# Optimization experiments

Hardware: AMD Instinct MI355X
Metric: run time of the kernel (lower is better)

## Reference

```python
import jax, jax.numpy as jnp
import numpy as np

TEMPERATURE = 0.1  # base_temperature=0.07 is unused in the original forward
K = 100            # hard-coded top-k in the original forward


def setup_inputs() -> dict:
    key = jax.random.key(0)
    k1, k2, k3, k4 = jax.random.split(key, 4)
    B, T, D, N = 16, 2048, 256, 128
    context_feature = jax.random.normal(k1, (B, T, D), dtype=jnp.float32)
    target_feature = jax.random.normal(k2, (B, T, D), dtype=jnp.float32)
    # torch.unique(mask_index): supply a pre-uniqued sorted 1D index set directly
    mask_index = jnp.sort(jax.random.permutation(k3, T)[:N]).astype(jnp.int32)
    phone_label = jax.random.randint(k4, (B, T), 0, 100, dtype=jnp.int32)
    return {"context_feature": context_feature, "target_feature": target_feature,
            "mask_index": mask_index, "phone_label": phone_label}


def reference(context_feature, target_feature, mask_index, phone_label):
    B, T, D = context_feature.shape
    N = mask_index.shape[0]

    # phone gather + inequality mask (BN, BT)
    phone_n = phone_label[:, mask_index].reshape(B * N)
    phone_t = phone_label.reshape(B * T)
    neq_mask = (phone_n[:, None] != phone_t[None, :]).astype(context_feature.dtype)

    anchors = context_feature[:, mask_index, :].reshape(B * N, D)
    negative = target_feature.reshape(B * T, D)
    positive = target_feature[:, mask_index, :].reshape(B * N, D)

    a_norm = jnp.linalg.norm(anchors, axis=1)   # (BN,)
    p_norm = jnp.linalg.norm(positive, axis=1)  # (BN,)
    n_norm = jnp.linalg.norm(negative, axis=1)  # (BT,)

    # numerator: original builds full (BN,BN) cosine matrix but only uses diag;
    # compute the diagonal directly (identical math, far less memory)
    cos_pos = jnp.sum(anchors * positive, axis=1) / (a_norm * p_norm)
    sim_numerator = jnp.exp(jnp.arccos(jnp.clip(cos_pos, -1.0, 1.0)) / TEMPERATURE)

    # denominator: (BN, BT) cosine -> acos -> exp -> mask -> top-k sum
    cos_neg = (anchors @ negative.T) / (a_norm[:, None] * n_norm[None, :])
    sim_den = jnp.exp(jnp.arccos(jnp.clip(cos_neg, -1.0, 1.0)) / TEMPERATURE) * neq_mask
    top_vals = jax.lax.top_k(sim_den, K)[0]          # == sort desc then take first K
    sim_den_final = top_vals.sum(axis=1)             # (BN,)

    logit = jnp.log(sim_numerator / sim_den_final)
    loss = (-1.0 / (N * B)) * logit.sum()
    return loss
```

## Files before the change

### kernel.cpp

```cpp
#include <hip/hip_runtime.h>
#include <math.h>

#define TT 2048
#define TD 256
#define BN 2048
#define BT 32768
#define KTOP 100
#define CAP 1024
#define LCAP 1024
#define THETA -0.15f
#define BROWS 128
#define SLICE 512
#define NITER 16
#define FSCALE 301.176470588f
#define GH 32

typedef __attribute__((ext_vector_type(8))) short short8v;
typedef __attribute__((ext_vector_type(4))) float float4v;

__device__ __forceinline__ unsigned short f2bf(float f) {
    unsigned u = __float_as_uint(f);
    u += 0x7fffu + ((u >> 16) & 1u);
    return (unsigned short)(u >> 16);
}

__device__ __forceinline__ int tile_off_us(int col, int l) {
    int ks = l >> 3;
    int g = (l >> 1) & 3;
    int e = (l & 1) * 4;
    return ((((col >> 4) * 8 + ks) * 4 + g) * 16 + (col & 15)) * 8 + e;
}

__global__ __launch_bounds__(256) void kinit(const float* __restrict__ ctx,
                                             const float* __restrict__ tgt,
                                             const int* __restrict__ mask_index,
                                             const int* __restrict__ phone,
                                             unsigned short* __restrict__ negT,
                                             unsigned short* __restrict__ ancT,
                                             float* __restrict__ acosP,
                                             int* __restrict__ phoneA,
                                             unsigned* __restrict__ ghp,
                                             int* __restrict__ cnt,
                                             int* __restrict__ flagA) {
    const int bid = blockIdx.x;
    const int tid = threadIdx.x;

    if (bid < 2048) {
        __shared__ float tile[16][257];
        __shared__ float psum[16][8];
        __shared__ float inv[16];
        const int cb = bid;
        for (int r = 0; r < 16; ++r)
            tile[r][tid] = tgt[((size_t)cb * 16 + r) * TD + tid];
        __syncthreads();
        if (tid < 128) {
            int row = tid >> 3, seg = tid & 7;
            float s = 0.f;
            for (int j = 0; j < 32; ++j) {
                float x = tile[row][seg * 32 + j];
                s += x * x;
            }
            psum[row][seg] = s;
        }
        __syncthreads();
        if (tid < 16) {
            float s = 0.f;
            for (int j = 0; j < 8; ++j) s += psum[tid][j];
            inv[tid] = 1.0f / sqrtf(s);
        }
        __syncthreads();
        const int col = tid & 15;
        const float iv = inv[col];
        unsigned short* out = negT + (size_t)cb * 4096;
#pragma unroll
        for (int half = 0; half < 2; ++half) {
            const int d0 = (tid >> 4) * 8 + half * 128;
            ushort4 o0, o1;
            o0.x = f2bf(tile[col][d0 + 0] * iv);
            o0.y = f2bf(tile[col][d0 + 1] * iv);
            o0.z = f2bf(tile[col][d0 + 2] * iv);
            o0.w = f2bf(tile[col][d0 + 3] * iv);
            o1.x = f2bf(tile[col][d0 + 4] * iv);
            o1.y = f2bf(tile[col][d0 + 5] * iv);
            o1.z = f2bf(tile[col][d0 + 6] * iv);
            o1.w = f2bf(tile[col][d0 + 7] * iv);
            *reinterpret_cast<ushort4*>(out + (size_t)(half * 256 + tid) * 8) = o0;
            *reinterpret_cast<ushort4*>(out + (size_t)(half * 256 + tid) * 8 + 4) = o1;
        }
        return;
    }
    if (bid < 2560) {
        const int r = (bid - 2048) * 4 + (tid >> 6);
        const int lane = tid & 63;
        const int b = r >> 7;
        const int n = r & 127;
        const int t = mask_index[n];
        const size_t base = ((size_t)b * TT + t) * TD;
        float4 a = *reinterpret_cast<const float4*>(ctx + base + lane * 4);
        float4 p = *reinterpret_cast<const float4*>(tgt + base + lane * 4);
        float sa = a.x * a.x + a.y * a.y + a.z * a.z + a.w * a.w;
        float sp = p.x * p.x + p.y * p.y + p.z * p.z + p.w * p.w;
        float dp = a.x * p.x + a.y * p.y + a.z * p.z + a.w * p.w;
        for (int off = 32; off > 0; off >>= 1) {
            sa += __shfl_down(sa, off, 64);
            sp += __shfl_down(sp, off, 64);
            dp += __shfl_down(dp, off, 64);
        }
        sa = __shfl(sa, 0, 64);
        sp = __shfl(sp, 0, 64);
        dp = __shfl(dp, 0, 64);
        const float an = sqrtf(sa);
        const float inva = 1.0f / an;
        if (lane == 0) {
            float cp = dp / (an * sqrtf(sp));
            cp = fminf(1.f, fmaxf(-1.f, cp));
            acosP[r] = acosf(cp) * 10.0f;
            phoneA[r] = phone[b * TT + t];
        }
        ushort4 o;
        o.x = f2bf(a.x * inva); o.y = f2bf(a.y * inva);
        o.z = f2bf(a.z * inva); o.w = f2bf(a.w * inva);
        *reinterpret_cast<ushort4*>(ancT + tile_off_us(r, lane)) = o;
        return;
    }
    if (bid < 2560 + GH) {
        __shared__ unsigned h[128];
        const int s = bid - 2560;
        if (tid < 128) h[tid] = 0u;
        __syncthreads();
        const int base = s * (BT / GH);
        for (int i = tid; i < BT / GH; i += 256)
            atomicAdd(&h[phone[base + i] & 127], 1u);
        __syncthreads();
        if (tid < 128) ghp[s * 128 + tid] = h[tid];
        return;
    }
    {
        const int i = (bid - 2592) * 256 + tid;
        if (i < BN) { cnt[i] = 0; flagA[i] = 0; }
    }
}

__global__ __launch_bounds__(512, 4) void kpass(const short8v* __restrict__ ancT8,
                                                const short8v* __restrict__ negT8,
                                                const int* __restrict__ phoneT,
                                                const int* __restrict__ phoneA,
                                                float* __restrict__ list,
                                                int* __restrict__ cnt,
                                                int* __restrict__ flag) {
    __shared__ float candV[LCAP];
    __shared__ int candR[LCAP];
    __shared__ int s_nc;
    const int tid = threadIdx.x;
    const int w = tid >> 6;
    const int lane = tid & 63;
    const int g = lane >> 4;
    const int c = lane & 15;
    const int wr = w >> 1;
    const int wc = w & 1;
    const int logical = (blockIdx.x & 7) * 128 + (blockIdx.x >> 3);
    const int ct = logical >> 4;
    const int rt = logical & 15;
    const int row0 = rt * BROWS;
    const int colbase = ct * SLICE;

    if (tid == 0) s_nc = 0;

    short8v af[2][8];
#pragma unroll
    for (int mt = 0; mt < 2; ++mt) {
        const int tile = rt * 8 + wr * 2 + mt;
#pragma unroll
        for (int ks = 0; ks < 8; ++ks)
            af[mt][ks] = ancT8[(tile * 8 + ks) * 64 + lane];
    }
    int phA_r[2][4];
#pragma unroll
    for (int mt = 0; mt < 2; ++mt)
#pragma unroll
        for (int j = 0; j < 4; ++j)
            phA_r[mt][j] = phoneA[row0 + wr * 32 + mt * 16 + g * 4 + j];
    __syncthreads();

#pragma unroll 2
    for (int it = 0; it < NITER; ++it) {
        const int cb = colbase + it * 32 + wc * 16;
        const int fb = (cb >> 4) * 8 * 64 + lane;
        short8v bf[8];
#pragma unroll
        for (int ks = 0; ks < 8; ++ks)
            bf[ks] = negT8[fb + ks * 64];
        const int ph = phoneT[cb + c];
        float4v acc0 = (float4v){0.f, 0.f, 0.f, 0.f};
        float4v acc1 = (float4v){0.f, 0.f, 0.f, 0.f};
        __builtin_amdgcn_s_setprio(1);
#pragma unroll
        for (int ks = 0; ks < 8; ++ks) {
            acc0 = __builtin_amdgcn_mfma_f32_16x16x32_bf16(af[0][ks], bf[ks], acc0, 0, 0, 0);
            acc1 = __builtin_amdgcn_mfma_f32_16x16x32_bf16(af[1][ks], bf[ks], acc1, 0, 0, 0);
        }
        __builtin_amdgcn_s_setprio(0);
#pragma unroll
        for (int j = 0; j < 4; ++j) {
            float v0 = fminf(1.f, fmaxf(-1.f, acc0[j]));
            if (v0 < THETA && ph != phA_r[0][j]) {
                int k = atomicAdd(&s_nc, 1);
                if (k < LCAP) {
                    candV[k] = v0;
                    candR[k] = row0 + wr * 32 + g * 4 + j;
                }
            }
            float v1 = fminf(1.f, fmaxf(-1.f, acc1[j]));
            if (v1 < THETA && ph != phA_r[1][j]) {
                int k = atomicAdd(&s_nc, 1);
                if (k < LCAP) {
                    candV[k] = v1;
                    candR[k] = row0 + wr * 32 + 16 + g * 4 + j;
                }
            }
        }
    }

    __syncthreads();
    const int nc = s_nc;
    if (nc > LCAP) {
        for (int i = tid; i < BROWS; i += 512) flag[row0 + i] = 1;
    } else {
        for (int i = tid; i < nc; i += 512) {
            const int r = candR[i];
            int idx = atomicAdd(&cnt[r], 1);
            if (idx < CAP) list[(size_t)r * CAP + idx] = candV[i];
        }
    }
}

__global__ __launch_bounds__(64) void kfinal(const float* __restrict__ list,
                                             const int* __restrict__ cnt,
                                             const int* __restrict__ phoneA,
                                             const unsigned* __restrict__ ghp,
                                             const float* __restrict__ acosP,
                                             float* __restrict__ logits,
                                             int* __restrict__ flag) {
    __shared__ float sl[CAP];
    __shared__ unsigned subh[256];
    __shared__ float l2[128];
    __shared__ int s_b, s_cum, s_l2c;
    const int row = blockIdx.x;
    const int lane = threadIdx.x;
    const int mp = phoneA[row] & 127;
    int un = BT;
    for (int s = 0; s < GH; ++s) un -= (int)ghp[s * 128 + mp];
    const int kp = un < KTOP ? un : KTOP;
    const int c = cnt[row];
    if (kp <= 0) { if (lane == 0) logits[row] = acosP[row]; return; }
    if (c < kp || c > CAP) { if (lane == 0) flag[row] = 1; return; }

    for (int i = lane; i < c; i += 64) sl[i] = list[(size_t)row * CAP + i];
    for (int i = lane; i < 256; i += 64) subh[i] = 0u;
    if (lane == 0) s_l2c = 0;
    __syncthreads();

    for (int i = lane; i < c; i += 64) {
        int sb = (int)((sl[i] + 1.0f) * FSCALE);
        sb = sb < 0 ? 0 : (sb > 255 ? 255 : sb);
        atomicAdd(&subh[sb], 1u);
    }
    __syncthreads();
    if (lane == 0) {
        unsigned cum = 0;
        int b = 0;
        for (; b < 256; ++b) {
            if (cum + subh[b] >= (unsigned)kp) break;
            cum += subh[b];
        }
        s_b = b > 255 ? 255 : b;
        s_cum = (int)cum;
    }
    __syncthreads();
    const int bs = s_b, cum = s_cum;

    float ls = 0.f;
    for (int i = lane; i < c; i += 64) {
        float v = sl[i];
        int sb = (int)((v + 1.0f) * FSCALE);
        sb = sb < 0 ? 0 : (sb > 255 ? 255 : sb);
        if (sb < bs) {
            ls += expf(acosf(fminf(1.f, fmaxf(-1.f, v))) * 10.0f);
        } else if (sb == bs) {
            int k = atomicAdd(&s_l2c, 1);
            if (k < 128) l2[k] = v;
        }
    }
#pragma unroll
    for (int off = 1; off < 64; off <<= 1) ls += __shfl_xor(ls, off, 64);
    __syncthreads();
    const int n2 = s_l2c;
    if (n2 > 128) { if (lane == 0) flag[row] = 1; return; }

    float den = ls;
    int rem = kp - cum;
    if (rem > n2) rem = n2;
    float v0 = lane < n2 ? l2[lane] : 1e30f;
    float v1 = lane + 64 < n2 ? l2[lane + 64] : 1e30f;
    for (int it = 0; it < rem; ++it) {
        float mv = fminf(v0, v1);
        int mi = (v1 < v0) ? lane + 64 : lane;
#pragma unroll
        for (int off = 1; off < 64; off <<= 1) {
            float ov = __shfl_xor(mv, off, 64);
            int oi = __shfl_xor(mi, off, 64);
            if (ov < mv || (ov == mv && oi < mi)) { mv = ov; mi = oi; }
        }
        den += expf(acosf(fminf(1.f, fmaxf(-1.f, mv))) * 10.0f);
        if (mi == lane) v0 = 1e30f;
        if (mi == lane + 64) v1 = 1e30f;
    }
    if (lane == 0) logits[row] = acosP[row] - logf(den);
}

__global__ __launch_bounds__(256) void kfallback(const float* __restrict__ ctx,
                                                 const float* __restrict__ tgt,
                                                 const int* __restrict__ mask_index,
                                                 const int* __restrict__ phone,
                                                 const int* __restrict__ flag,
                                                 const unsigned* __restrict__ ghp,
                                                 const float* __restrict__ acosP,
                                                 float* __restrict__ logits) {
    const int row = blockIdx.x;
    if (!flag[row]) return;
    __shared__ float anc[TD];
    __shared__ float redf[256];
    __shared__ int redi[256];
    __shared__ unsigned hist[2048];
    __shared__ float lst[512];
    __shared__ int s_b, s_cum, s_lc;
    const int tid = threadIdx.x;
    const int b = row >> 7;
    const int t = mask_index[row & 127];
    const int mp = phone[b * TT + t];

    {
        float x = ctx[((size_t)b * TT + t) * TD + tid];
        redf[tid] = x * x;
        anc[tid] = x;
        __syncthreads();
        for (int s = 128; s > 0; s >>= 1) {
            if (tid < s) redf[tid] += redf[tid + s];
            __syncthreads();
        }
        float inv = 1.0f / sqrtf(redf[0]);
        __syncthreads();
        anc[tid] *= inv;
    }
    for (int i = tid; i < 2048; i += 256) hist[i] = 0u;
    if (tid == 0) s_lc = 0;
    __syncthreads();

    int un = BT;
    for (int s = 0; s < GH; ++s) un -= (int)ghp[s * 128 + (mp & 127)];
    const int kp = un < KTOP ? un : KTOP;
    if (kp <= 0) { if (tid == 0) logits[row] = acosP[row]; return; }

    for (int col = tid; col < BT; col += 256) {
        if (phone[col] == mp) continue;
        const float* nr = tgt + (size_t)col * TD;
        float dot = 0.f, sq = 0.f;
        for (int d = 0; d < TD; d += 4) {
            float4 v = *reinterpret_cast<const float4*>(nr + d);
            dot += anc[d] * v.x + anc[d + 1] * v.y + anc[d + 2] * v.z + anc[d + 3] * v.w;
            sq += v.x * v.x + v.y * v.y + v.z * v.z + v.w * v.w;
        }
        float cv = fminf(1.f, fmaxf(-1.f, dot / sqrtf(sq)));
        int bb = (int)((cv + 1.0f) * 1024.0f);
        bb = bb > 2047 ? 2047 : bb;
        atomicAdd(&hist[bb], 1u);
    }
    __syncthreads();
    if (tid == 0) {
        unsigned cum = 0;
        int bb = 0;
        for (; bb < 2048; ++bb) {
            if (cum + hist[bb] >= (unsigned)kp) break;
            cum += hist[bb];
        }
        s_b = bb > 2047 ? 2047 : bb;
        s_cum = (int)cum;
    }
    __syncthreads();
    const int bs = s_b;

    float ls = 0.f;
    for (int col = tid; col < BT; col += 256) {
        if (phone[col] == mp) continue;
        const float* nr = tgt + (size_t)col * TD;
        float dot = 0.f, sq = 0.f;
        for (int d = 0; d < TD; d += 4) {
            float4 v = *reinterpret_cast<const float4*>(nr + d);
            dot += anc[d] * v.x + anc[d + 1] * v.y + anc[d + 2] * v.z + anc[d + 3] * v.w;
            sq += v.x * v.x + v.y * v.y + v.z * v.z + v.w * v.w;
        }
        float cv = fminf(1.f, fmaxf(-1.f, dot / sqrtf(sq)));
        int bb = (int)((cv + 1.0f) * 1024.0f);
        bb = bb > 2047 ? 2047 : bb;
        if (bb < bs) {
            ls += expf(acosf(cv) * 10.0f);
        } else if (bb == bs) {
            int k = atomicAdd(&s_lc, 1);
            if (k < 512) lst[k] = cv;
        }
    }
    redf[tid] = ls;
    __syncthreads();
    for (int s = 128; s > 0; s >>= 1) {
        if (tid < s) redf[tid] += redf[tid + s];
        __syncthreads();
    }
    float den = redf[0];
    __syncthreads();

    int lc = s_lc < 512 ? s_lc : 512;
    int rem = kp - s_cum;
    if (rem > lc) rem = lc;
    for (int it = 0; it < rem; ++it) {
        float mv = 1e30f;
        int mi = -1;
        for (int i = tid; i < lc; i += 256) {
            if (lst[i] < mv) { mv = lst[i]; mi = i; }
        }
        redf[tid] = mv;
        redi[tid] = mi;
        __syncthreads();
        for (int s = 128; s > 0; s >>= 1) {
            if (tid < s && (redf[tid + s] < redf[tid] ||
                            (redf[tid + s] == redf[tid] && redi[tid + s] >= 0 &&
                             (redi[tid] < 0 || redi[tid + s] < redi[tid])))) {
                redf[tid] = redf[tid + s];
                redi[tid] = redi[tid + s];
            }
            __syncthreads();
        }
        if (tid == 0) {
            den += expf(acosf(fminf(1.f, fmaxf(-1.f, redf[0]))) * 10.0f);
            if (redi[0] >= 0) lst[redi[0]] = 1e30f;
            redf[0] = den;
        }
        __syncthreads();
        den = redf[0];
        __syncthreads();
    }
    if (tid == 0) logits[row] = acosP[row] - logf(den);
}

__global__ __launch_bounds__(256) void kloss(const float* __restrict__ logits,
                                             float* __restrict__ out) {
    __shared__ float red[256];
    int tid = threadIdx.x;
    float s = 0.f;
    for (int i = tid; i < BN; i += 256) s += logits[i];
    red[tid] = s;
    __syncthreads();
    for (int st = 128; st > 0; st >>= 1) {
        if (tid < st) red[tid] += red[tid + st];
        __syncthreads();
    }
    if (tid == 0) out[0] = -red[0] / (float)BN;
}

extern "C" void kernel_launch(void* const* d_in, const int* in_sizes, int n_in,
                              void* d_out, int out_size, void* d_ws, size_t ws_size,
                              hipStream_t stream) {
    (void)in_sizes; (void)n_in; (void)out_size; (void)ws_size;
    const float* ctx   = (const float*)d_in[0];
    const float* tgt   = (const float*)d_in[1];
    const int*   mask  = (const int*)d_in[2];
    const int*   phone = (const int*)d_in[3];
    float* out = (float*)d_out;

    char* p = (char*)d_ws;
    unsigned short* negT = (unsigned short*)p;            p += (size_t)BT * TD * 2;
    unsigned short* ancT = (unsigned short*)p;            p += (size_t)BN * TD * 2;
    float* acosP  = (float*)p;                            p += (size_t)BN * 4;
    int*   phoneA = (int*)p;                              p += (size_t)BN * 4;
    int*   cntA   = (int*)p;                              p += (size_t)BN * 4;
    int*   flagA  = (int*)p;                              p += (size_t)BN * 4;
    unsigned* ghp = (unsigned*)p;                         p += (size_t)GH * 128 * 4;
    float* listA  = (float*)p;                            p += (size_t)BN * CAP * 4;
    float* logits = (float*)p;                            p += (size_t)BN * 4;

    kinit<<<2600, 256, 0, stream>>>(ctx, tgt, mask, phone, negT, ancT,
                                    acosP, phoneA, ghp, cntA, flagA);
    kpass<<<1024, 512, 0, stream>>>((const short8v*)ancT, (const short8v*)negT,
                                    phone, phoneA, listA, cntA, flagA);
    kfinal<<<BN, 64, 0, stream>>>(listA, cntA, phoneA, ghp, acosP, logits, flagA);
    kfallback<<<BN, 256, 0, stream>>>(ctx, tgt, mask, phone, flagA, ghp, acosP, logits);
    kloss<<<1, 256, 0, stream>>>(logits, out);
}
```

Measured before the change: 132.9 us.

## Retile kpass: stage anchor tile in LDS via direct loads, widen column tiles

Changes the kpass tiling from 128 rows x 512 columns with 8 waves holding anchor fragments in registers to 64 rows x 1024 columns with 4 waves. The anchor tile is copied into LDS with global_load_lds, and each wave reads it from there for all four 16-row subtiles while reusing two negative fragments from registers. This raises reuse of each negative load and lowers register pressure, at the cost of LDS reads in the inner MFMA loop and more LDS per block. It also drops the redundant upper clamp, since only values below a negative threshold are kept.

```diff
diff --git a/kernel.cpp b/kernel.cpp
--- a/kernel.cpp
+++ b/kernel.cpp
@@ -9,9 +9,9 @@
 #define CAP 1024
 #define LCAP 1024
 #define THETA -0.15f
-#define BROWS 128
-#define SLICE 512
-#define NITER 16
+#define BROWS 64
+#define BCOLS 1024
+#define NITER 8
 #define FSCALE 301.176470588f
 #define GH 32
 
@@ -29,6 +29,12 @@
     int g = (l >> 1) & 3;
     int e = (l & 1) * 4;
     return ((((col >> 4) * 8 + ks) * 4 + g) * 16 + (col & 15)) * 8 + e;
+}
+
+__device__ __forceinline__ void gload16(const void* g, void* l) {
+    __builtin_amdgcn_global_load_lds(
+        (const __attribute__((address_space(1))) unsigned*)g,
+        (__attribute__((address_space(3))) unsigned*)l, 16, 0, 0);
 }
 
 __global__ __launch_bounds__(256) void kinit(const float* __restrict__ ctx,
@@ -141,13 +147,14 @@
     }
 }
 
-__global__ __launch_bounds__(512, 4) void kpass(const short8v* __restrict__ ancT8,
+__global__ __launch_bounds__(256, 3) void kpass(const short8v* __restrict__ ancT8,
                                                 const short8v* __restrict__ negT8,
                                                 const int* __restrict__ phoneT,
                                                 const int* __restrict__ phoneA,
                                                 float* __restrict__ list,
                                                 int* __restrict__ cnt,
                                                 int* __restrict__ flag) {
+    __shared__ short8v aLDS[2048];
     __shared__ float candV[LCAP];
     __shared__ int candR[LCAP];
     __shared__ int s_nc;
@@ -156,77 +163,79 @@
     const int lane = tid & 63;
     const int g = lane >> 4;
     const int c = lane & 15;
-    const int wr = w >> 1;
-    const int wc = w & 1;
     const int logical = (blockIdx.x & 7) * 128 + (blockIdx.x >> 3);
-    const int ct = logical >> 4;
-    const int rt = logical & 15;
+    const int ct = logical >> 5;
+    const int rt = logical & 31;
     const int row0 = rt * BROWS;
-    const int colbase = ct * SLICE;
-
+    const int colbase = ct * BCOLS;
+
+    {
+        const char* asrc = (const char*)(ancT8 + (size_t)rt * 2048);
+#pragma unroll
+        for (int i = 0; i < 8; ++i)
+            gload16(asrc + i * 4096 + tid * 16, (char*)aLDS + i * 4096 + tid * 16);
+    }
     if (tid == 0) s_nc = 0;
-
-    short8v af[2][8];
-#pragma unroll
-    for (int mt = 0; mt < 2; ++mt) {
-        const int tile = rt * 8 + wr * 2 + mt;
-#pragma unroll
-        for (int ks = 0; ks < 8; ++ks)
-            af[mt][ks] = ancT8[(tile * 8 + ks) * 64 + lane];
-    }
-    int phA_r[2][4];
-#pragma unroll
-    for (int mt = 0; mt < 2; ++mt)
+    int phA_r[4][4];
+#pragma unroll
+    for (int t = 0; t < 4; ++t)
 #pragma unroll
         for (int j = 0; j < 4; ++j)
-            phA_r[mt][j] = phoneA[row0 + wr * 32 + mt * 16 + g * 4 + j];
-    __syncthreads();
-
-#pragma unroll 2
+            phA_r[t][j] = phoneA[row0 + t * 16 + g * 4 + j];
+    __syncthreads();
+
+#pragma unroll 1
     for (int it = 0; it < NITER; ++it) {
-        const int cb = colbase + it * 32 + wc * 16;
-        const int fb = (cb >> 4) * 8 * 64 + lane;
-        short8v bf[8];
-#pragma unroll
-        for (int ks = 0; ks < 8; ++ks)
-            bf[ks] = negT8[fb + ks * 64];
-        const int ph = phoneT[cb + c];
-        float4v acc0 = (float4v){0.f, 0.f, 0.f, 0.f};
-        float4v acc1 = (float4v){0.f, 0.f, 0.f, 0.f};
-        __builtin_amdgcn_s_setprio(1);
+        const int cb = colbase + it * 128 + w * 32;
+        const int fb = (cb >> 4) * 512 + lane;
+        short8v bf[2][8];
 #pragma unroll
         for (int ks = 0; ks < 8; ++ks) {
-            acc0 = __builtin_amdgcn_mfma_f32_16x16x32_bf16(af[0][ks], bf[ks], acc0, 0, 0, 0);
-            acc1 = __builtin_amdgcn_mfma_f32_16x16x32_bf16(af[1][ks], bf[ks], acc1, 0, 0, 0);
-        }
-        __builtin_amdgcn_s_setprio(0);
-#pragma unroll
-        for (int j = 0; j < 4; ++j) {
-            float v0 = fminf(1.f, fmaxf(-1.f, acc0[j]));
-            if (v0 < THETA && ph != phA_r[0][j]) {
-                int k = atomicAdd(&s_nc, 1);
-                if (k < LCAP) {
-                    candV[k] = v0;
-                    candR[k] = row0 + wr * 32 + g * 4 + j;
+            bf[0][ks] = negT8[fb + ks * 64];
+            bf[1][ks] = negT8[fb + 512 + ks * 64];
+        }
+        const int ph0 = phoneT[cb + c];
+        const int ph1 = phoneT[cb + 16 + c];
+#pragma unroll
+        for (int t = 0; t < 4; ++t) {
+            float4v acc0 = (float4v){0.f, 0.f, 0.f, 0.f};
+            float4v acc1 = (float4v){0.f, 0.f, 0.f, 0.f};
+            __builtin_amdgcn_s_setprio(1);
+#pragma unroll
+            for (int ks = 0; ks < 8; ++ks) {
+                short8v af = aLDS[(t * 8 + ks) * 64 + lane];
+                acc0 = __builtin_amdgcn_mfma_f32_16x16x32_bf16(af, bf[0][ks], acc0, 0, 0, 0);
+                acc1 = __builtin_amdgcn_mfma_f32_16x16x32_bf16(af, bf[1][ks], acc1, 0, 0, 0);
+            }
+            __builtin_amdgcn_s_setprio(0);
+#pragma unroll
+            for (int j = 0; j < 4; ++j) {
+                float v0 = acc0[j];
+                if (v0 < THETA && ph0 != phA_r[t][j]) {
+                    int k = atomicAdd(&s_nc, 1);
+                    if (k < LCAP) {
+                        candV[k] = fmaxf(-1.f, v0);
+                        candR[k] = row0 + t * 16 + g * 4 + j;
+                    }
+                }
+                float v1 = acc1[j];
+                if (v1 < THETA && ph1 != phA_r[t][j]) {
+                    int k = atomicAdd(&s_nc, 1);
+                    if (k < LCAP) {
+                        candV[k] = fmaxf(-1.f, v1);
+                        candR[k] = row0 + t * 16 + g * 4 + j;
+                    }
                 }
             }
-            float v1 = fminf(1.f, fmaxf(-1.f, acc1[j]));
-            if (v1 < THETA && ph != phA_r[1][j]) {
-                int k = atomicAdd(&s_nc, 1);
-                if (k < LCAP) {
-                    candV[k] = v1;
-                    candR[k] = row0 + wr * 32 + 16 + g * 4 + j;
-                }
-            }
         }
     }
 
     __syncthreads();
     const int nc = s_nc;
     if (nc > LCAP) {
-        for (int i = tid; i < BROWS; i += 512) flag[row0 + i] = 1;
+        for (int i = tid; i < BROWS; i += 256) flag[row0 + i] = 1;
     } else {
-        for (int i = tid; i < nc; i += 512) {
+        for (int i = tid; i < nc; i += 256) {
             const int r = candR[i];
             int idx = atomicAdd(&cnt[r], 1);
             if (idx < CAP) list[(size_t)r * CAP + idx] = candV[i];
@@ -489,7 +498,7 @@
 
     kinit<<<2600, 256, 0, stream>>>(ctx, tgt, mask, phone, negT, ancT,
                                     acosP, phoneA, ghp, cntA, flagA);
-    kpass<<<1024, 512, 0, stream>>>((const short8v*)ancT, (const short8v*)negT,
+    kpass<<<1024, 256, 0, stream>>>((const short8v*)ancT, (const short8v*)negT,
                                     phone, phoneA, listA, cntA, flagA);
     kfinal<<<BN, 64, 0, stream>>>(listA, cntA, phoneA, ghp, acosP, logits, flagA);
     kfallback<<<BN, 256, 0, stream>>>(ctx, tgt, mask, phone, flagA, ghp, acosP, logits);
```

Measured after the change: 144.0 us. 1.08x slower.

## Replace shared-memory atomic candidate append with per-wave ballot compaction

Applied to the files above, without the earlier changes.

The candidate-filter kernel now compacts threshold-passing cosine values per wavefront using ballot plus popcount, writing into a per-wave LDS buffer. This replaces the block-wide atomic counter on shared memory. Blocks shrink to 256 threads covering 64 rows, with twice as many blocks. Overflow is flagged per 32-row wave group instead of per 128-row block, and the clamp before the comparison is dropped. The aim is to remove contended LDS atomics, at the cost of a smaller per-wave capacity that may send more rows to the fallback path.

```diff
diff --git a/kernel.cpp b/kernel.cpp
--- a/kernel.cpp
+++ b/kernel.cpp
@@ -7,10 +7,10 @@
 #define BT 32768
 #define KTOP 100
 #define CAP 1024
-#define LCAP 1024
+#define WCAP 256
 #define THETA -0.15f
-#define BROWS 128
-#define SLICE 512
+#define BROWS 64
+#define BCOLS 512
 #define NITER 16
 #define FSCALE 301.176470588f
 #define GH 32
@@ -141,16 +141,15 @@
     }
 }
 
-__global__ __launch_bounds__(512, 4) void kpass(const short8v* __restrict__ ancT8,
+__global__ __launch_bounds__(256, 4) void kpass(const short8v* __restrict__ ancT8,
                                                 const short8v* __restrict__ negT8,
                                                 const int* __restrict__ phoneT,
                                                 const int* __restrict__ phoneA,
                                                 float* __restrict__ list,
                                                 int* __restrict__ cnt,
                                                 int* __restrict__ flag) {
-    __shared__ float candV[LCAP];
-    __shared__ int candR[LCAP];
-    __shared__ int s_nc;
+    __shared__ float candV[4][WCAP];
+    __shared__ int candR[4][WCAP];
     const int tid = threadIdx.x;
     const int w = tid >> 6;
     const int lane = tid & 63;
@@ -158,18 +157,17 @@
     const int c = lane & 15;
     const int wr = w >> 1;
     const int wc = w & 1;
-    const int logical = (blockIdx.x & 7) * 128 + (blockIdx.x >> 3);
-    const int ct = logical >> 4;
-    const int rt = logical & 15;
+    const unsigned long long lmask_lt = (1ull << lane) - 1ull;
+    const int logical = (blockIdx.x & 7) * 256 + (blockIdx.x >> 3);
+    const int ct = logical >> 5;
+    const int rt = logical & 31;
     const int row0 = rt * BROWS;
-    const int colbase = ct * SLICE;
-
-    if (tid == 0) s_nc = 0;
+    const int colbase = ct * BCOLS;
 
     short8v af[2][8];
 #pragma unroll
     for (int mt = 0; mt < 2; ++mt) {
-        const int tile = rt * 8 + wr * 2 + mt;
+        const int tile = rt * 4 + wr * 2 + mt;
 #pragma unroll
         for (int ks = 0; ks < 8; ++ks)
             af[mt][ks] = ancT8[(tile * 8 + ks) * 64 + lane];
@@ -180,12 +178,13 @@
 #pragma unroll
         for (int j = 0; j < 4; ++j)
             phA_r[mt][j] = phoneA[row0 + wr * 32 + mt * 16 + g * 4 + j];
-    __syncthreads();
+
+    int k0 = 0;
 
 #pragma unroll 2
     for (int it = 0; it < NITER; ++it) {
         const int cb = colbase + it * 32 + wc * 16;
-        const int fb = (cb >> 4) * 8 * 64 + lane;
+        const int fb = (cb >> 4) * 512 + lane;
         short8v bf[8];
 #pragma unroll
         for (int ks = 0; ks < 8; ++ks)
@@ -202,34 +201,37 @@
         __builtin_amdgcn_s_setprio(0);
 #pragma unroll
         for (int j = 0; j < 4; ++j) {
-            float v0 = fminf(1.f, fmaxf(-1.f, acc0[j]));
-            if (v0 < THETA && ph != phA_r[0][j]) {
-                int k = atomicAdd(&s_nc, 1);
-                if (k < LCAP) {
-                    candV[k] = v0;
-                    candR[k] = row0 + wr * 32 + g * 4 + j;
+            bool p0 = (acc0[j] < THETA) && (ph != phA_r[0][j]);
+            unsigned long long m0 = __ballot(p0);
+            if (p0) {
+                int pos = k0 + __popcll(m0 & lmask_lt);
+                if (pos < WCAP) {
+                    candV[w][pos] = acc0[j];
+                    candR[w][pos] = row0 + wr * 32 + g * 4 + j;
                 }
             }
-            float v1 = fminf(1.f, fmaxf(-1.f, acc1[j]));
-            if (v1 < THETA && ph != phA_r[1][j]) {
-                int k = atomicAdd(&s_nc, 1);
-                if (k < LCAP) {
-                    candV[k] = v1;
-                    candR[k] = row0 + wr * 32 + 16 + g * 4 + j;
+            k0 += __popcll(m0);
+            bool p1 = (acc1[j] < THETA) && (ph != phA_r[1][j]);
+            unsigned long long m1 = __ballot(p1);
+            if (p1) {
+                int pos = k0 + __popcll(m1 & lmask_lt);
+                if (pos < WCAP) {
+                    candV[w][pos] = acc1[j];
+                    candR[w][pos] = row0 + wr * 32 + 16 + g * 4 + j;
                 }
             }
-        }
-    }
-
-    __syncthreads();
-    const int nc = s_nc;
-    if (nc > LCAP) {
-        for (int i = tid; i < BROWS; i += 512) flag[row0 + i] = 1;
+            k0 += __popcll(m1);
+        }
+    }
+
+    __syncthreads();
+    if (k0 > WCAP) {
+        if (lane < 32) flag[row0 + wr * 32 + lane] = 1;
     } else {
-        for (int i = tid; i < nc; i += 512) {
-            const int r = candR[i];
+        for (int i = lane; i < k0; i += 64) {
+            const int r = candR[w][i];
             int idx = atomicAdd(&cnt[r], 1);
-            if (idx < CAP) list[(size_t)r * CAP + idx] = candV[i];
+            if (idx < CAP) list[(size_t)r * CAP + idx] = candV[w][i];
         }
     }
 }
@@ -489,7 +491,7 @@
 
     kinit<<<2600, 256, 0, stream>>>(ctx, tgt, mask, phone, negT, ancT,
                                     acosP, phoneA, ghp, cntA, flagA);
-    kpass<<<1024, 512, 0, stream>>>((const short8v*)ancT, (const short8v*)negT,
+    kpass<<<2048, 256, 0, stream>>>((const short8v*)ancT, (const short8v*)negT,
                                     phone, phoneA, listA, cntA, flagA);
     kfinal<<<BN, 64, 0, stream>>>(listA, cntA, phoneA, ghp, acosP, logits, flagA);
     kfallback<<<BN, 256, 0, stream>>>(ctx, tgt, mask, phone, flagA, ghp, acosP, logits);
```

After: 177.4 us. +33.5%, slower.
